# Kernel tuning notes

Measured on AMD Instinct MI355X. Metric: run time of the kernel, lower is better.

## Reference

```python
import jax, jax.numpy as jnp
import numpy as np

B, S, E, H = 2, 2048, 2048, 16
D = E // H  # head_dim = 128


def setup_inputs() -> dict:
    key = jax.random.key(0)
    ks = jax.random.split(key, 11)
    scale = 1.0 / np.sqrt(E)
    return {
        "query": jax.random.normal(ks[0], (B, S, E), dtype=jnp.float32),
        "key_in": jax.random.normal(ks[1], (B, S, E), dtype=jnp.float32),
        "value": jax.random.normal(ks[2], (B, S, E), dtype=jnp.float32),
        "Wq": jax.random.normal(ks[3], (E, E), dtype=jnp.float32) * scale,
        "bq": jnp.zeros((E,), dtype=jnp.float32),
        "Wk": jax.random.normal(ks[4], (E, E), dtype=jnp.float32) * scale,
        "bk": jnp.zeros((E,), dtype=jnp.float32),
        "Wv": jax.random.normal(ks[5], (E, E), dtype=jnp.float32) * scale,
        "bv": jnp.zeros((E,), dtype=jnp.float32),
        "Wo": jax.random.normal(ks[6], (E, E), dtype=jnp.float32) * scale,
        "bo": jnp.zeros((E,), dtype=jnp.float32),
    }


def reference(query, key_in, value, Wq, bq, Wk, bk, Wv, bv, Wo, bo):
    # Linear projections then split heads: (B,S,E) -> (B,H,S,D)
    def proj(x, W, b):
        y = x @ W + b
        return y.reshape(B, S, H, D).transpose(0, 2, 1, 3)

    Q = proj(query, Wq, bq)
    K = proj(key_in, Wk, bk)
    V = proj(value, Wv, bv)

    # scores: (B,H,S,S)
    scores = jnp.einsum('bhqd,bhkd->bhqk', Q, K) / jnp.sqrt(jnp.float32(D))
    attn = jax.nn.softmax(scores, axis=-1)
    # attn output: (B,H,S,D) -> (B,S,E)
    out = jnp.einsum('bhqk,bhkd->bhqd', attn, V)
    out = out.transpose(0, 2, 1, 3).reshape(B, S, E)
    return out @ Wo + bo
```

## Files before the change

kernel.cpp:

```cpp
#include <hip/hip_runtime.h>
#include <hip/hip_bf16.h>

typedef __bf16 bf16;
typedef __bf16 bf16x8 __attribute__((ext_vector_type(8)));
typedef float f32x4 __attribute__((ext_vector_type(4)));

constexpr int kE = 2048;
constexpr int kS = 2048;
constexpr int kB = 2;
constexpr int kH = 16;
constexpr int kD = 128;
constexpr int kM = kB * kS;
constexpr float kQScale = 0.12751743f;

#define MFMA_BF16(A, B, C) __builtin_amdgcn_mfma_f32_16x16x32_bf16((A), (B), (C), 0, 0, 0)

__device__ __forceinline__ void async_ld16(const void* gsrc, void* ldst) {
  __builtin_amdgcn_global_load_lds(
      (__attribute__((address_space(1))) void*)(gsrc),
      (__attribute__((address_space(3))) void*)(ldst), 16, 0, 0);
}

__global__ __launch_bounds__(256) void cvt_kernel(
    const float* __restrict__ Xq, const float* __restrict__ Xk,
    const float* __restrict__ Xv, bf16* __restrict__ Y) {
  const int z = blockIdx.y;
  const float* X = (z == 0) ? Xq : (z == 1) ? Xk : Xv;
  bf16* Yz = Y + (size_t)z * kM * kE;
  size_t i = ((size_t)blockIdx.x * 256 + threadIdx.x) * 8;
  float4 v0 = *(const float4*)(X + i);
  float4 v1 = *(const float4*)(X + i + 4);
  bf16x8 hv;
  hv[0] = (bf16)v0.x; hv[1] = (bf16)v0.y; hv[2] = (bf16)v0.z; hv[3] = (bf16)v0.w;
  hv[4] = (bf16)v1.x; hv[5] = (bf16)v1.y; hv[6] = (bf16)v1.z; hv[7] = (bf16)v1.w;
  *(bf16x8*)(Yz + i) = hv;
}

__global__ __launch_bounds__(256) void wt_kernel(
    const float* __restrict__ Wq, const float* __restrict__ Wk,
    const float* __restrict__ Wv, const float* __restrict__ Wo,
    bf16* __restrict__ WT) {
  __shared__ bf16 tl[64][72];
  const int z = blockIdx.z;
  const float* W = (z == 0) ? Wq : (z == 1) ? Wk : (z == 2) ? Wv : Wo;
  const int n0 = blockIdx.x * 64, k0 = blockIdx.y * 64;
  const int t = threadIdx.x;

  {
    const int k = t >> 2, nq = (t & 3) * 16;
    const float* src = &W[(size_t)(k0 + k) * kE + n0 + nq];
#pragma unroll
    for (int u = 0; u < 4; ++u) {
      float4 v = *(const float4*)(src + u * 4);
      tl[nq + u * 4 + 0][k] = (bf16)v.x;
      tl[nq + u * 4 + 1][k] = (bf16)v.y;
      tl[nq + u * 4 + 2][k] = (bf16)v.z;
      tl[nq + u * 4 + 3][k] = (bf16)v.w;
    }
  }
  __syncthreads();
  {
    const int n = t >> 2, seg = (t & 3) * 16;
    bf16x8 a = *(const bf16x8*)&tl[n][seg];
    bf16x8 b2 = *(const bf16x8*)&tl[n][seg + 8];
    bf16* dst = &WT[(size_t)(z * kE + n0 + n) * kE + k0 + seg];
    *(bf16x8*)dst = a;
    *(bf16x8*)(dst + 8) = b2;
  }
}

__global__ __launch_bounds__(256) void gemm_qkv_kernel(
    const bf16* __restrict__ Xb, const bf16* __restrict__ WT,
    const float* __restrict__ bq, const float* __restrict__ bk,
    const float* __restrict__ bv, bf16* __restrict__ Qb,
    bf16* __restrict__ Kb, bf16* __restrict__ Vb) {
  __shared__ alignas(16) bf16 As[128 * 64];
  __shared__ alignas(16) bf16 Bs[128 * 64];

  const int z = blockIdx.z;
  const bf16* A = Xb + (size_t)z * kM * kE;
  const float* bias = (z == 0) ? bq : (z == 1) ? bk : bv;
  bf16* dstbuf = (z == 0) ? Qb : (z == 1) ? Kb : Vb;
  const float oscale = (z == 0) ? kQScale : 1.0f;
  const bf16* Bt = WT + (size_t)z * kE * kE;

  const int n0 = blockIdx.x * 128;
  const int m0 = blockIdx.y * 128;
  const int t = threadIdx.x;
  const int lane = t & 63;
  const int w = t >> 6;
  const int ln = lane & 15;
  const int qd = lane >> 4;
  const int wm = w >> 1, wn = w & 1;

  const f32x4 fzero = {0.f, 0.f, 0.f, 0.f};
  f32x4 acc[4][4];
#pragma unroll
  for (int i = 0; i < 4; ++i)
#pragma unroll
    for (int j = 0; j < 4; ++j) acc[i][j] = fzero;

  for (int k0 = 0; k0 < kE; k0 += 64) {
    __syncthreads();
#pragma unroll
    for (int i = 0; i < 4; ++i) {
      int c = t + i * 256;
      int row = c >> 3;
      int slot = c & 7;
      int g = slot ^ (row & 7);
      async_ld16(&A[(size_t)(m0 + row) * kE + k0 + g * 8],
                 &As[(size_t)(w * 64 + i * 256) * 8]);
    }
#pragma unroll
    for (int i = 0; i < 4; ++i) {
      int c = t + i * 256;
      int row = c >> 3;
      int slot = c & 7;
      int g = slot ^ (row & 7);
      async_ld16(&Bt[(size_t)(n0 + row) * kE + k0 + g * 8],
                 &Bs[(size_t)(w * 64 + i * 256) * 8]);
    }
    __syncthreads();
#pragma unroll
    for (int ks = 0; ks < 2; ++ks) {
      bf16x8 af[4], bfv[4];
#pragma unroll
      for (int i = 0; i < 4; ++i) {
        int row = wm * 64 + i * 16 + ln;
        int slot = (ks * 4 + qd) ^ (ln & 7);
        af[i] = *(const bf16x8*)&As[row * 64 + slot * 8];
      }
#pragma unroll
      for (int j = 0; j < 4; ++j) {
        int row = wn * 64 + j * 16 + ln;
        int slot = (ks * 4 + qd) ^ (ln & 7);
        bfv[j] = *(const bf16x8*)&Bs[row * 64 + slot * 8];
      }
#pragma unroll
      for (int i = 0; i < 4; ++i)
#pragma unroll
        for (int j = 0; j < 4; ++j)
          acc[i][j] = MFMA_BF16(af[i], bfv[j], acc[i][j]);
    }
  }

#pragma unroll
  for (int i = 0; i < 4; ++i) {
    int mbase = m0 + wm * 64 + i * 16 + qd * 4;
#pragma unroll
    for (int j = 0; j < 4; ++j) {
      int n = n0 + wn * 64 + j * 16 + ln;
      float bn = bias[n];
      int h = n >> 7, d = n & 127;
#pragma unroll
      for (int r = 0; r < 4; ++r) {
        int mm = mbase + r;
        int bb = mm >> 11, ss = mm & (kS - 1);
        dstbuf[((size_t)(bb * kH + h) * kS + ss) * kD + d] =
            (bf16)((acc[i][j][r] + bn) * oscale);
      }
    }
  }
}

__global__ __launch_bounds__(256) void vtrans_kernel(
    const bf16* __restrict__ Vb, bf16* __restrict__ VT) {
  __shared__ bf16 tl[64][72];
  const int bh = blockIdx.z;
  const int s0 = blockIdx.x * 64, d0 = blockIdx.y * 64;
  const bf16* src = Vb + ((size_t)bh * kS + s0) * kD + d0;
  bf16* dst = VT + ((size_t)bh * kD + d0) * kS + s0;
  const int t = threadIdx.x;
#pragma unroll
  for (int i = 0; i < 2; ++i) {
    int c = t + i * 256;
    int s = c >> 3, dc = (c & 7) * 8;
    bf16x8 v = *(const bf16x8*)&src[(size_t)s * kD + dc];
#pragma unroll
    for (int e = 0; e < 8; ++e) tl[dc + e][s] = v[e];
  }
  __syncthreads();
#pragma unroll
  for (int i = 0; i < 2; ++i) {
    int c = t + i * 256;
    int d = c >> 3, sc = (c & 7) * 8;
    bf16x8 v = *(const bf16x8*)&tl[d][sc];
    *(bf16x8*)&dst[(size_t)d * kS + sc] = v;
  }
}

__global__ __launch_bounds__(256) void attn_kernel(
    const bf16* __restrict__ Qb, const bf16* __restrict__ Kb,
    const bf16* __restrict__ VTb, bf16* __restrict__ AO) {
  __shared__ alignas(16) bf16 Kt[64 * 128];
  __shared__ alignas(16) bf16 Vt[128 * 64];
  __shared__ alignas(16) bf16 Pl[4][16 * 64];

  const int b = blockIdx.z, h = blockIdx.y;
  const int q0 = blockIdx.x * 64;
  const int t = threadIdx.x, lane = t & 63, w = t >> 6;
  const int ln = lane & 15, qd = lane >> 4;

  const bf16* Qh = Qb + (size_t)(b * kH + h) * kS * kD;
  const bf16* Kh = Kb + (size_t)(b * kH + h) * kS * kD;
  const bf16* Vh = VTb + (size_t)(b * kH + h) * kD * kS;

  bf16x8 qf[4];
  {
    int qr = q0 + w * 16 + ln;
#pragma unroll
    for (int f = 0; f < 4; ++f)
      qf[f] = *(const bf16x8*)&Qh[(size_t)qr * kD + f * 32 + qd * 8];
  }

  const f32x4 fzero = {0.f, 0.f, 0.f, 0.f};
  f32x4 o[8];
#pragma unroll
  for (int dt = 0; dt < 8; ++dt) o[dt] = fzero;
  float lsum[4] = {0.f, 0.f, 0.f, 0.f};

  for (int kc = 0; kc < kS; kc += 64) {
    __syncthreads();
#pragma unroll
    for (int i = 0; i < 4; ++i) {
      int c = t + i * 256;
      int row = c >> 4;
      int slot = c & 15;
      int g = slot ^ (row & 15);
      async_ld16(&Kh[(size_t)(kc + row) * kD + g * 8],
                 &Kt[(size_t)(w * 64 + i * 256) * 8]);
    }
#pragma unroll
    for (int i = 0; i < 4; ++i) {
      int c = t + i * 256;
      int row = c >> 3;
      int slot = c & 7;
      int g = slot ^ (row & 7);
      async_ld16(&Vh[(size_t)row * kS + kc + g * 8],
                 &Vt[(size_t)(w * 64 + i * 256) * 8]);
    }
    __syncthreads();

    f32x4 s[4];
#pragma unroll
    for (int nt = 0; nt < 4; ++nt) s[nt] = fzero;
#pragma unroll
    for (int nt = 0; nt < 4; ++nt) {
      int row = nt * 16 + ln;
#pragma unroll
      for (int f = 0; f < 4; ++f) {
        int slot = (f * 4 + qd) ^ ln;
        bf16x8 kfv = *(const bf16x8*)&Kt[row * 128 + slot * 8];
        s[nt] = MFMA_BF16(qf[f], kfv, s[nt]);
      }
    }

#pragma unroll
    for (int nt = 0; nt < 4; ++nt)
#pragma unroll
      for (int r = 0; r < 4; ++r) {
        float p = __builtin_amdgcn_exp2f(s[nt][r]);
        lsum[r] += p;
        int prow = qd * 4 + r;
        int gchunk = nt * 2 + (ln >> 3);
        int slot = gchunk ^ (prow & 7);
        Pl[w][prow * 64 + slot * 8 + (ln & 7)] = (bf16)p;
      }
    asm volatile("s_waitcnt lgkmcnt(0)" ::: "memory");

    bf16x8 pf[2];
#pragma unroll
    for (int kf = 0; kf < 2; ++kf) {
      int slot = (kf * 4 + qd) ^ (ln & 7);
      pf[kf] = *(const bf16x8*)&Pl[w][ln * 64 + slot * 8];
    }
#pragma unroll
    for (int dt = 0; dt < 8; ++dt) {
      int row = dt * 16 + ln;
#pragma unroll
      for (int kf = 0; kf < 2; ++kf) {
        int slot = (kf * 4 + qd) ^ (ln & 7);
        bf16x8 vv = *(const bf16x8*)&Vt[row * 64 + slot * 8];
        o[dt] = MFMA_BF16(pf[kf], vv, o[dt]);
      }
    }
  }

#pragma unroll
  for (int r = 0; r < 4; ++r) {
    float l = lsum[r];
    l += __shfl_xor(l, 1);
    l += __shfl_xor(l, 2);
    l += __shfl_xor(l, 4);
    l += __shfl_xor(l, 8);
    float inv = 1.f / l;
    int srow = q0 + w * 16 + qd * 4 + r;
    bf16* dst = AO + (size_t)(b * kS + srow) * kE + h * kD;
#pragma unroll
    for (int dt = 0; dt < 8; ++dt)
      dst[dt * 16 + ln] = (bf16)(o[dt][r] * inv);
  }
}

__global__ __launch_bounds__(256) void gemm_out_kernel(
    const bf16* __restrict__ A, const bf16* __restrict__ Bt,
    const float* __restrict__ bias, float* __restrict__ out) {
  __shared__ alignas(16) bf16 As[128 * 64];
  __shared__ alignas(16) bf16 Bs[128 * 64];

  const int n0 = blockIdx.x * 128;
  const int m0 = blockIdx.y * 128;
  const int t = threadIdx.x;
  const int lane = t & 63;
  const int w = t >> 6;
  const int ln = lane & 15;
  const int qd = lane >> 4;
  const int wm = w >> 1, wn = w & 1;

  const f32x4 fzero = {0.f, 0.f, 0.f, 0.f};
  f32x4 acc[4][4];
#pragma unroll
  for (int i = 0; i < 4; ++i)
#pragma unroll
    for (int j = 0; j < 4; ++j) acc[i][j] = fzero;

  for (int k0 = 0; k0 < kE; k0 += 64) {
    __syncthreads();
#pragma unroll
    for (int i = 0; i < 4; ++i) {
      int c = t + i * 256;
      int row = c >> 3;
      int slot = c & 7;
      int g = slot ^ (row & 7);
      async_ld16(&A[(size_t)(m0 + row) * kE + k0 + g * 8],
                 &As[(size_t)(w * 64 + i * 256) * 8]);
    }
#pragma unroll
    for (int i = 0; i < 4; ++i) {
      int c = t + i * 256;
      int row = c >> 3;
      int slot = c & 7;
      int g = slot ^ (row & 7);
      async_ld16(&Bt[(size_t)(n0 + row) * kE + k0 + g * 8],
                 &Bs[(size_t)(w * 64 + i * 256) * 8]);
    }
    __syncthreads();
#pragma unroll
    for (int ks = 0; ks < 2; ++ks) {
      bf16x8 af[4], bfv[4];
#pragma unroll
      for (int i = 0; i < 4; ++i) {
        int row = wm * 64 + i * 16 + ln;
        int slot = (ks * 4 + qd) ^ (ln & 7);
        af[i] = *(const bf16x8*)&As[row * 64 + slot * 8];
      }
#pragma unroll
      for (int j = 0; j < 4; ++j) {
        int row = wn * 64 + j * 16 + ln;
        int slot = (ks * 4 + qd) ^ (ln & 7);
        bfv[j] = *(const bf16x8*)&Bs[row * 64 + slot * 8];
      }
#pragma unroll
      for (int i = 0; i < 4; ++i)
#pragma unroll
        for (int j = 0; j < 4; ++j)
          acc[i][j] = MFMA_BF16(af[i], bfv[j], acc[i][j]);
    }
  }

#pragma unroll
  for (int i = 0; i < 4; ++i) {
    int mbase = m0 + wm * 64 + i * 16 + qd * 4;
#pragma unroll
    for (int j = 0; j < 4; ++j) {
      int n = n0 + wn * 64 + j * 16 + ln;
      float bn = bias[n];
#pragma unroll
      for (int r = 0; r < 4; ++r) {
        int mm = mbase + r;
        out[(size_t)mm * kE + n] = acc[i][j][r] + bn;
      }
    }
  }
}

extern "C" void kernel_launch(void* const* d_in, const int* in_sizes, int n_in,
                              void* d_out, int out_size, void* d_ws,
                              size_t ws_size, hipStream_t stream) {
  const float* query  = (const float*)d_in[0];
  const float* key_in = (const float*)d_in[1];
  const float* value  = (const float*)d_in[2];
  const float* Wq = (const float*)d_in[3];
  const float* bq = (const float*)d_in[4];
  const float* Wk = (const float*)d_in[5];
  const float* bk = (const float*)d_in[6];
  const float* Wv = (const float*)d_in[7];
  const float* bv = (const float*)d_in[8];
  const float* Wo = (const float*)d_in[9];
  const float* bo = (const float*)d_in[10];
  float* out = (float*)d_out;

  const size_t szWT  = (size_t)4 * kE * kE;
  const size_t szAct = (size_t)kM * kE;
  const size_t need = (szWT + 7 * szAct) * sizeof(bf16);
  if (ws_size < need) return;

  bf16* WT  = (bf16*)d_ws;
  bf16* Qb  = WT + szWT;
  bf16* Kb  = Qb + szAct;
  bf16* VTb = Kb + szAct;
  bf16* AO  = VTb + szAct;
  bf16* Xb  = AO + szAct;
  bf16* Vb  = AO;

  wt_kernel<<<dim3(kE / 64, kE / 64, 4), 256, 0, stream>>>(
      Wq, Wk, Wv, Wo, WT);
  cvt_kernel<<<dim3(kM * kE / 8 / 256, 3), 256, 0, stream>>>(
      query, key_in, value, Xb);
  gemm_qkv_kernel<<<dim3(kE / 128, kM / 128, 3), 256, 0, stream>>>(
      Xb, WT, bq, bk, bv, Qb, Kb, Vb);
  vtrans_kernel<<<dim3(kS / 64, kD / 64, kB * kH), 256, 0, stream>>>(
      Vb, VTb);
  attn_kernel<<<dim3(kS / 64, kH, kB), 256, 0, stream>>>(Qb, Kb, VTb, AO);
  gemm_out_kernel<<<dim3(kE / 128, kM / 128), 256, 0, stream>>>(
      AO, WT + (size_t)3 * kE * kE, bo, out);
}
```

Before: 466.1 us.

## Rewrite QKV GEMM as 256x256 tile, 8-wave, double-buffered pingpong pipeline

Replaces the 128x128 single-buffered QKV projection GEMM with a 256x256 tile kernel using 8 waves and double-buffered LDS. Global-to-LDS async loads for the next K tile are interleaved with MFMA quadrants, using fine-grained barriers, explicit vmcnt waits and s_setprio around the MFMA sections. Workgroup indices are swizzled across the three projections for L2 locality. The aim is to hide load latency and raise arithmetic intensity. In exchange it uses much more LDS and registers, and relies on hand-tuned wait counts whose correctness is fragile.

```diff
diff --git a/kernel.cpp b/kernel.cpp
--- a/kernel.cpp
+++ b/kernel.cpp
@@ -69,87 +69,181 @@
   }
 }
 
-__global__ __launch_bounds__(256) void gemm_qkv_kernel(
+
+#define LD_A(dst, Asb, mh)                                            \
+  do {                                                                \
+    _Pragma("unroll") for (int m_ = 0; m_ < 4; ++m_) {                \
+      int row_ = wm * 128 + ((mh) * 4 + m_) * 16 + ln;                \
+      _Pragma("unroll") for (int k_ = 0; k_ < 2; ++k_) {              \
+        int slot_ = (k_ * 4 + qd) ^ (ln & 7);                         \
+        dst[m_][k_] = *(const bf16x8*)&(Asb)[row_ * 64 + slot_ * 8];  \
+      }                                                               \
+    }                                                                 \
+  } while (0)
+
+#define LD_B(dst, Bsb, nh)                                            \
+  do {                                                                \
+    _Pragma("unroll") for (int n_ = 0; n_ < 2; ++n_) {                \
+      int row_ = wn * 64 + ((nh) * 2 + n_) * 16 + ln;                 \
+      _Pragma("unroll") for (int k_ = 0; k_ < 2; ++k_) {              \
+        int slot_ = (k_ * 4 + qd) ^ (ln & 7);                         \
+        dst[n_][k_] = *(const bf16x8*)&(Bsb)[row_ * 64 + slot_ * 8];  \
+      }                                                               \
+    }                                                                 \
+  } while (0)
+
+#define QMFMA(am, bn, mh, nh)                                         \
+  do {                                                                \
+    _Pragma("unroll") for (int m_ = 0; m_ < 4; ++m_)                  \
+    _Pragma("unroll") for (int n_ = 0; n_ < 2; ++n_)                  \
+    _Pragma("unroll") for (int k_ = 0; k_ < 2; ++k_)                  \
+      acc[(mh) * 4 + m_][(nh) * 2 + n_] = MFMA_BF16(                  \
+          am[m_][k_], bn[n_][k_], acc[(mh) * 4 + m_][(nh) * 2 + n_]); \
+  } while (0)
+
+#define P_BAR1                                  \
+  do {                                          \
+    asm volatile("" ::: "memory");              \
+    __builtin_amdgcn_s_barrier();               \
+    asm volatile("" ::: "memory");              \
+  } while (0)
+#define P_END                                             \
+  do {                                                    \
+    asm volatile("s_waitcnt lgkmcnt(0)" ::: "memory");    \
+    __builtin_amdgcn_s_barrier();                         \
+    asm volatile("" ::: "memory");                        \
+  } while (0)
+
+__global__ __launch_bounds__(512, 2) void gemm_qkv8_kernel(
     const bf16* __restrict__ Xb, const bf16* __restrict__ WT,
     const float* __restrict__ bq, const float* __restrict__ bk,
     const float* __restrict__ bv, bf16* __restrict__ Qb,
     bf16* __restrict__ Kb, bf16* __restrict__ Vb) {
-  __shared__ alignas(16) bf16 As[128 * 64];
-  __shared__ alignas(16) bf16 Bs[128 * 64];
-
-  const int z = blockIdx.z;
-  const bf16* A = Xb + (size_t)z * kM * kE;
+  __shared__ alignas(16) bf16 As[2][256 * 64];
+  __shared__ alignas(16) bf16 Bs[2][256 * 64];
+
+  const int wg = blockIdx.x;
+  const int swz = (wg & 7) * 48 + (wg >> 3);
+  const int z = swz >> 7;
+  const int rem = swz & 127;
+  const int m0 = (rem >> 3) * 256;
+  const int n0 = (rem & 7) * 256;
+
+  const bf16* A  = Xb + (size_t)z * kM * kE + (size_t)m0 * kE;
+  const bf16* Bt = WT + (size_t)z * kE * kE + (size_t)n0 * kE;
   const float* bias = (z == 0) ? bq : (z == 1) ? bk : bv;
   bf16* dstbuf = (z == 0) ? Qb : (z == 1) ? Kb : Vb;
   const float oscale = (z == 0) ? kQScale : 1.0f;
-  const bf16* Bt = WT + (size_t)z * kE * kE;
-
-  const int n0 = blockIdx.x * 128;
-  const int m0 = blockIdx.y * 128;
+
   const int t = threadIdx.x;
-  const int lane = t & 63;
-  const int w = t >> 6;
-  const int ln = lane & 15;
-  const int qd = lane >> 4;
-  const int wm = w >> 1, wn = w & 1;
+  const int lane = t & 63, w = t >> 6;
+  const int ln = lane & 15, qd = lane >> 4;
+  const int wm = w >> 2, wn = w & 3;
+
+  auto stage = [&](const bf16* gt, bf16* lt, int half) {
+#pragma unroll
+    for (int i = 0; i < 2; ++i) {
+      int c = i * 512 + w * 64 + lane;
+      int row = c >> 3, slot = c & 7, g = slot ^ (row & 7);
+      async_ld16(&gt[(size_t)(half * 128 + row) * kE + g * 8],
+                 &lt[half * 8192 + (i * 512 + w * 64) * 8]);
+    }
+  };
 
   const f32x4 fzero = {0.f, 0.f, 0.f, 0.f};
-  f32x4 acc[4][4];
-#pragma unroll
-  for (int i = 0; i < 4; ++i)
+  f32x4 acc[8][4];
+#pragma unroll
+  for (int i = 0; i < 8; ++i)
 #pragma unroll
     for (int j = 0; j < 4; ++j) acc[i][j] = fzero;
 
-  for (int k0 = 0; k0 < kE; k0 += 64) {
-    __syncthreads();
-#pragma unroll
-    for (int i = 0; i < 4; ++i) {
-      int c = t + i * 256;
-      int row = c >> 3;
-      int slot = c & 7;
-      int g = slot ^ (row & 7);
-      async_ld16(&A[(size_t)(m0 + row) * kE + k0 + g * 8],
-                 &As[(size_t)(w * 64 + i * 256) * 8]);
-    }
-#pragma unroll
-    for (int i = 0; i < 4; ++i) {
-      int c = t + i * 256;
-      int row = c >> 3;
-      int slot = c & 7;
-      int g = slot ^ (row & 7);
-      async_ld16(&Bt[(size_t)(n0 + row) * kE + k0 + g * 8],
-                 &Bs[(size_t)(w * 64 + i * 256) * 8]);
-    }
-    __syncthreads();
-#pragma unroll
-    for (int ks = 0; ks < 2; ++ks) {
-      bf16x8 af[4], bfv[4];
-#pragma unroll
-      for (int i = 0; i < 4; ++i) {
-        int row = wm * 64 + i * 16 + ln;
-        int slot = (ks * 4 + qd) ^ (ln & 7);
-        af[i] = *(const bf16x8*)&As[row * 64 + slot * 8];
-      }
-#pragma unroll
-      for (int j = 0; j < 4; ++j) {
-        int row = wn * 64 + j * 16 + ln;
-        int slot = (ks * 4 + qd) ^ (ln & 7);
-        bfv[j] = *(const bf16x8*)&Bs[row * 64 + slot * 8];
-      }
-#pragma unroll
-      for (int i = 0; i < 4; ++i)
-#pragma unroll
-        for (int j = 0; j < 4; ++j)
-          acc[i][j] = MFMA_BF16(af[i], bfv[j], acc[i][j]);
-    }
-  }
-
-#pragma unroll
-  for (int i = 0; i < 4; ++i) {
-    int mbase = m0 + wm * 64 + i * 16 + qd * 4;
-#pragma unroll
-    for (int j = 0; j < 4; ++j) {
-      int n = n0 + wn * 64 + j * 16 + ln;
+  bf16x8 aL[4][2], aH[4][2], bA[2][2], bB[2][2];
+
+  stage(Bt, Bs[0], 0);
+  stage(Bt, Bs[0], 1);
+  stage(A, As[0], 0);
+  stage(A, As[0], 1);
+  stage(Bt + 64, Bs[1], 0);
+  stage(Bt + 64, Bs[1], 1);
+  asm volatile("s_waitcnt vmcnt(4)" ::: "memory");
+  __builtin_amdgcn_s_barrier();
+  asm volatile("" ::: "memory");
+
+#pragma unroll 1
+  for (int u = 0; u < 16; ++u) {
+    const bf16* AgO = A + (size_t)(2 * u + 1) * 64;
+    int tE = 2 * u + 2; if (tE > 31) tE = 31;
+    int tO = 2 * u + 3; if (tO > 31) tO = 31;
+    const bf16* AgE2 = A  + (size_t)tE * 64;
+    const bf16* BgE2 = Bt + (size_t)tE * 64;
+    const bf16* BgO2 = Bt + (size_t)tO * 64;
+
+    LD_A(aL, As[0], 0);
+    LD_B(bA, Bs[0], 0);
+    stage(AgO, As[1], 0);
+    P_BAR1;
+    __builtin_amdgcn_s_setprio(1);
+    QMFMA(aL, bA, 0, 0);
+    __builtin_amdgcn_s_setprio(0);
+    P_END;
+    LD_B(bB, Bs[0], 1);
+    stage(AgO, As[1], 1);
+    P_BAR1;
+    __builtin_amdgcn_s_setprio(1);
+    QMFMA(aL, bB, 0, 1);
+    __builtin_amdgcn_s_setprio(0);
+    P_END;
+    LD_A(aH, As[0], 1);
+    stage(BgE2, Bs[0], 0);
+    P_BAR1;
+    __builtin_amdgcn_s_setprio(1);
+    QMFMA(aH, bA, 1, 0);
+    __builtin_amdgcn_s_setprio(0);
+    P_END;
+    stage(BgE2, Bs[0], 1);
+    P_BAR1;
+    __builtin_amdgcn_s_setprio(1);
+    QMFMA(aH, bB, 1, 1);
+    __builtin_amdgcn_s_setprio(0);
+    asm volatile("s_waitcnt vmcnt(4)" ::: "memory");
+    P_END;
+    LD_A(aL, As[1], 0);
+    LD_B(bA, Bs[1], 0);
+    stage(AgE2, As[0], 0);
+    P_BAR1;
+    __builtin_amdgcn_s_setprio(1);
+    QMFMA(aL, bA, 0, 0);
+    __builtin_amdgcn_s_setprio(0);
+    P_END;
+    LD_B(bB, Bs[1], 1);
+    stage(AgE2, As[0], 1);
+    P_BAR1;
+    __builtin_amdgcn_s_setprio(1);
+    QMFMA(aL, bB, 0, 1);
+    __builtin_amdgcn_s_setprio(0);
+    P_END;
+    LD_A(aH, As[1], 1);
+    stage(BgO2, Bs[1], 0);
+    P_BAR1;
+    __builtin_amdgcn_s_setprio(1);
+    QMFMA(aH, bA, 1, 0);
+    __builtin_amdgcn_s_setprio(0);
+    P_END;
+    stage(BgO2, Bs[1], 1);
+    P_BAR1;
+    __builtin_amdgcn_s_setprio(1);
+    QMFMA(aH, bB, 1, 1);
+    __builtin_amdgcn_s_setprio(0);
+    asm volatile("s_waitcnt vmcnt(4)" ::: "memory");
+    P_END;
+  }
+
+#pragma unroll
+  for (int mf = 0; mf < 8; ++mf) {
+    int mbase = m0 + wm * 128 + mf * 16 + qd * 4;
+#pragma unroll
+    for (int nf = 0; nf < 4; ++nf) {
+      int n = n0 + wn * 64 + nf * 16 + ln;
       float bn = bias[n];
       int h = n >> 7, d = n & 127;
 #pragma unroll
@@ -157,7 +251,7 @@
         int mm = mbase + r;
         int bb = mm >> 11, ss = mm & (kS - 1);
         dstbuf[((size_t)(bb * kH + h) * kS + ss) * kD + d] =
-            (bf16)((acc[i][j][r] + bn) * oscale);
+            (bf16)((acc[mf][nf][r] + bn) * oscale);
       }
     }
   }
@@ -417,7 +511,7 @@
       Wq, Wk, Wv, Wo, WT);
   cvt_kernel<<<dim3(kM * kE / 8 / 256, 3), 256, 0, stream>>>(
       query, key_in, value, Xb);
-  gemm_qkv_kernel<<<dim3(kE / 128, kM / 128, 3), 256, 0, stream>>>(
+  gemm_qkv8_kernel<<<dim3(3 * (kM / 256) * (kE / 256)), 512, 0, stream>>>(
       Xb, WT, bq, bk, bv, Qb, Kb, Vb);
   vtrans_kernel<<<dim3(kS / 64, kD / 64, kB * kH), 256, 0, stream>>>(
       Vb, VTb);
```

After: 470.0 us. Within noise of the previous version (+0.8%).
